# Kernel tuning notes

Measured on AMD Instinct MI355X. Metric: run time of the kernel, lower is better.

## Reference

```python
import jax, jax.numpy as jnp
import numpy as np

EMBED_DIM = 1024
NUM_HEADS = 16
HEAD_DIM = EMBED_DIM // NUM_HEADS
WINDOW = 3
N_RAND = 3
BLOCK = 64
BATCH = 2
SEQ = 2048


def _bigbird_mask(seq_len: int) -> np.ndarray:
    """Global + sliding-window + random block mask. True = attend.
    Deterministic (fixed numpy seed) stand-in for np.random.choice in the
    original; the mask is data-independent so it is a compile-time constant."""
    nb = -(-seq_len // BLOCK)  # ceil division
    mask = np.zeros((seq_len, seq_len), dtype=bool)
    g = min(BLOCK, seq_len)
    mask[:g, :] = True  # global rows
    mask[:, :g] = True  # global cols
    blk = np.arange(seq_len) // BLOCK
    # sliding window: block distance <= WINDOW (matches start/end block loop)
    mask |= np.abs(blk[:, None] - blk[None, :]) <= WINDOW
    rng = np.random.RandomState(0)
    for b in range(1, nb):
        avail = [x for x in range(1, nb) if abs(x - b) > WINDOW]
        if avail:
            sel = rng.choice(avail, size=min(N_RAND, len(avail)), replace=False)
            s0, s1 = b * BLOCK, min(seq_len, (b + 1) * BLOCK)
            for rb in sel:
                mask[s0:s1, rb * BLOCK:min(seq_len, (rb + 1) * BLOCK)] = True
    return mask


def setup_inputs() -> dict:
    key = jax.random.key(0)
    ks = jax.random.split(key, 9)
    E = EMBED_DIM
    std = E ** -0.5
    return {
        "hidden_states": jax.random.normal(ks[0], (BATCH, SEQ, E), jnp.float32),
        "wq": jax.random.normal(ks[1], (E, E), jnp.float32) * std,
        "bq": jnp.zeros((E,), jnp.float32),
        "wk": jax.random.normal(ks[2], (E, E), jnp.float32) * std,
        "bk": jnp.zeros((E,), jnp.float32),
        "wv": jax.random.normal(ks[3], (E, E), jnp.float32) * std,
        "bv": jnp.zeros((E,), jnp.float32),
        "wo": jax.random.normal(ks[4], (E, E), jnp.float32) * std,
        "bo": jnp.zeros((E,), jnp.float32),
    }


def reference(hidden_states, wq, bq, wk, bk, wv, bv, wo, bo):
    B, S, E = hidden_states.shape
    D = HEAD_DIM
    scale = D ** -0.5

    def proj(w, b):  # (B,S,E) -> (B,H,S,D)
        return (hidden_states @ w.T + b).reshape(B, S, NUM_HEADS, D).transpose(0, 2, 1, 3)

    q = proj(wq, bq)
    k = proj(wk, bk)
    v = proj(wv, bv)
    scores = jnp.einsum('bhqd,bhkd->bhqk', q, k) * scale  # dense, masked post-hoc (as in source)
    mask = jnp.asarray(_bigbird_mask(S))
    scores = jnp.where(mask[None, None, :, :], scores, -jnp.inf)
    attn = jax.nn.softmax(scores, axis=-1)
    out = jnp.einsum('bhqk,bhkd->bhqd', attn, v)
    out = out.transpose(0, 2, 1, 3).reshape(B, S, E)
    return out @ wo.T + bo
```

## Files before the change

### kernel.cpp

```cpp
#include <hip/hip_runtime.h>
#include <cstdint>
#include <math.h>


#define DEVI __device__ __forceinline__

typedef __bf16 bf16x8 __attribute__((ext_vector_type(8)));
typedef float floatx4 __attribute__((ext_vector_type(4)));
typedef unsigned short u16x8 __attribute__((ext_vector_type(8)));
typedef unsigned short u16x4 __attribute__((ext_vector_type(4)));
typedef unsigned short ushort_t;

typedef const __attribute__((address_space(1))) void* gptr_as1;
typedef __attribute__((address_space(3))) void* lptr_as3;

DEVI ushort_t f2bf(float f) {
  unsigned u = __float_as_uint(f);
  unsigned r = ((u >> 16) & 1u) + 0x7fffu;
  return (ushort_t)((u + r) >> 16);
}

DEVI void lds_load16(void* lds, const void* g) {
  __builtin_amdgcn_global_load_lds((gptr_as1)g, (lptr_as3)lds, 16, 0, 0);
}

DEVI floatx4 mfma16(bf16x8 a, bf16x8 b, floatx4 c) {
  return __builtin_amdgcn_mfma_f32_16x16x32_bf16(a, b, c, 0, 0, 0);
}

#define BARR() do { asm volatile("" ::: "memory"); \
                    __builtin_amdgcn_s_barrier();  \
                    asm volatile("" ::: "memory"); } while (0)
#define LGKM0() asm volatile("s_waitcnt lgkmcnt(0)" ::: "memory")
#define VMC(N) asm volatile("s_waitcnt vmcnt(" #N ")" ::: "memory")

struct MTState { unsigned mt[624]; int mti; };

constexpr unsigned mt_next(MTState& s) {
  if (s.mti >= 624) {
    for (int k = 0; k < 624; ++k) {
      unsigned y = (s.mt[k] & 0x80000000u) | (s.mt[(k + 1) % 624] & 0x7fffffffu);
      unsigned v = s.mt[(k + 397) % 624] ^ (y >> 1);
      if (y & 1u) v ^= 0x9908b0dfu;
      s.mt[k] = v;
    }
    s.mti = 0;
  }
  unsigned y = s.mt[s.mti++];
  y ^= y >> 11;
  y ^= (y << 7) & 0x9d2c5680u;
  y ^= (y << 15) & 0xefc60000u;
  y ^= y >> 18;
  return y;
}

constexpr unsigned mt_interval(MTState& s, unsigned mx) {
  if (mx == 0u) return 0u;
  unsigned msk = mx;
  msk |= msk >> 1; msk |= msk >> 2; msk |= msk >> 4; msk |= msk >> 8; msk |= msk >> 16;
  unsigned v = mt_next(s) & msk;
  while (v > mx) v = mt_next(s) & msk;
  return v;
}

struct MaskPack { unsigned char list[32][32]; int cnt[32]; };

constexpr MaskPack make_pack() {
  unsigned char m[32][32] = {};
  for (int i = 0; i < 32; ++i)
    for (int j = 0; j < 32; ++j) {
      int d = i - j; if (d < 0) d = -d;
      m[i][j] = (i == 0 || j == 0 || d <= 3) ? (unsigned char)1 : (unsigned char)0;
    }
  MTState st{};
  st.mt[0] = 0u;
  for (int i = 1; i < 624; ++i)
    st.mt[i] = 1812433253u * (st.mt[i - 1] ^ (st.mt[i - 1] >> 30)) + (unsigned)i;
  st.mti = 624;
  for (int b = 1; b < 32; ++b) {
    int avail[32] = {}; int n = 0;
    for (int x = 1; x < 32; ++x) {
      int d = x - b; if (d < 0) d = -d;
      if (d > 3) avail[n++] = x;
    }
    if (n == 0) continue;
    int perm[32] = {};
    for (int i = 0; i < n; ++i) perm[i] = i;
    for (int i = n - 1; i > 0; --i) {
      unsigned j = mt_interval(st, (unsigned)i);
      int t = perm[i]; perm[i] = perm[(int)j]; perm[(int)j] = t;
    }
    int take = n < 3 ? n : 3;
    for (int s = 0; s < take; ++s) m[b][avail[perm[s]]] = 1;
  }
  MaskPack P{};
  for (int i = 0; i < 32; ++i) {
    int c = 0;
    for (int j = 0; j < 32; ++j)
      if (m[i][j]) P.list[i][c++] = (unsigned char)j;
    P.cnt[i] = c;
  }
  return P;
}

__constant__ MaskPack MP = make_pack();

__global__ __launch_bounds__(256) void cvt_all(
    const float* __restrict__ hs, const float* __restrict__ wq,
    const float* __restrict__ wk, const float* __restrict__ wv,
    const float* __restrict__ wo,
    ushort_t* __restrict__ hs_bf, ushort_t* __restrict__ wq_bf,
    ushort_t* __restrict__ wk_bf, ushort_t* __restrict__ wv_bf,
    ushort_t* __restrict__ wo_bf) {
  const int i = blockIdx.x * 256 + threadIdx.x;
  const float* s;
  ushort_t* d;
  int j;
  if (i < 1048576) {
    s = hs; d = hs_bf; j = i;
  } else {
    const int t = (i - 1048576) >> 18;
    j = (i - 1048576) & 262143;
    s = t == 0 ? wq : (t == 1 ? wk : (t == 2 ? wv : wo));
    d = t == 0 ? wq_bf : (t == 1 ? wk_bf : (t == 2 ? wv_bf : wo_bf));
  }
  const float4 f = ((const float4*)s)[j];
  u16x4 o;
  o.x = f2bf(f.x); o.y = f2bf(f.y); o.z = f2bf(f.z); o.w = f2bf(f.w);
  ((u16x4*)d)[j] = o;
}

DEVI void stage_half(ushort_t* ldsb, const ushort_t* g, int w, int l) {
  lds_load16(ldsb + w * 1024 + l * 8, g);
  lds_load16(ldsb + w * 1024 + 512 + l * 8, g + 8192);
}

DEVI void rdA(bf16x8 (&a)[4][2], const ushort_t* base, int wm, int li, int quad) {
#pragma unroll
  for (int mi = 0; mi < 4; ++mi) {
    const int rh = wm * 64 + mi * 16 + li;
    const int sw = rh & 7;
#pragma unroll
    for (int ks = 0; ks < 2; ++ks)
      a[mi][ks] = *(const bf16x8*)(base + rh * 64 + (((ks * 4 + quad) ^ sw) << 3));
  }
}

DEVI void rdB(bf16x8 (&b)[2][2], const ushort_t* base, int wn, int li, int quad) {
#pragma unroll
  for (int ni = 0; ni < 2; ++ni) {
    const int rh = wn * 32 + ni * 16 + li;
    const int sw = rh & 7;
#pragma unroll
    for (int ks = 0; ks < 2; ++ks)
      b[ni][ks] = *(const bf16x8*)(base + rh * 64 + (((ks * 4 + quad) ^ sw) << 3));
  }
}

DEVI void mm16(floatx4 (&c)[4][2], const bf16x8 (&a)[4][2], const bf16x8 (&b)[2][2]) {
  __builtin_amdgcn_s_setprio(1);
#pragma unroll
  for (int ks = 0; ks < 2; ++ks)
#pragma unroll
    for (int mi = 0; mi < 4; ++mi)
#pragma unroll
      for (int ni = 0; ni < 2; ++ni)
        c[mi][ni] = mfma16(a[mi][ks], b[ni][ks], c[mi][ni]);
  __builtin_amdgcn_s_setprio(0);
}

__global__ __launch_bounds__(512, 2) void gemm_qkv_fused(
    const ushort_t* __restrict__ A,
    const ushort_t* __restrict__ W0, const ushort_t* __restrict__ W1,
    const ushort_t* __restrict__ W2,
    const float* __restrict__ bq, const float* __restrict__ bk,
    const float* __restrict__ bv,
    ushort_t* __restrict__ Qo, ushort_t* __restrict__ Ko,
    ushort_t* __restrict__ Vt) {
  __shared__ alignas(16) ushort_t LDS[2][2][2][8192];
  const int tid = threadIdx.x;
  const int w = tid >> 6, l = tid & 63, quad = l >> 4, li = l & 15;
  const int wm = w >> 2, wn = w & 3;
  const int bid = blockIdx.x;
  const int swz = (bid & 7) * 24 + (bid >> 3);
  const int m0 = (swz / 12) << 8;
  const int n0g = (swz % 12) << 8;
  const int z = n0g >> 10, n0l = n0g & 1023;
  const ushort_t* Bw = z == 0 ? W0 : (z == 1 ? W1 : W2);
  const float* bias = z == 0 ? bq : (z == 1 ? bk : bv);

  const int rst = w * 16 + (l >> 3);
  const int cst = ((l & 7) ^ (l >> 3)) << 3;
  const ushort_t* gA = A + (size_t)(m0 + rst) * 1024 + cst;
  const ushort_t* gB = Bw + (size_t)(n0l + rst) * 1024 + cst;

  const floatx4 fz = {0.0f, 0.0f, 0.0f, 0.0f};
  floatx4 acc[2][2][4][2];
#pragma unroll
  for (int qm = 0; qm < 2; ++qm)
#pragma unroll
    for (int qn = 0; qn < 2; ++qn)
#pragma unroll
      for (int mi = 0; mi < 4; ++mi)
#pragma unroll
        for (int ni = 0; ni < 2; ++ni) acc[qm][qn][mi][ni] = fz;

  bf16x8 a[4][2], b0[2][2], b1[2][2];

  stage_half(&LDS[0][0][0][0], gA, w, l);
  stage_half(&LDS[0][0][1][0], gA + 131072, w, l);
  stage_half(&LDS[0][1][0][0], gB, w, l);
  stage_half(&LDS[0][1][1][0], gB + 131072, w, l);
  stage_half(&LDS[1][0][0][0], gA + 64, w, l);
  stage_half(&LDS[1][1][0][0], gB + 64, w, l);
  stage_half(&LDS[1][1][1][0], gB + 131072 + 64, w, l);
  VMC(6);
  BARR();

#pragma unroll 1
  for (int it = 0; it < 8; ++it) {
    const bool pf = (it < 7);
    const int o_cy = (2 * it + 1) * 64;
    const int o_x = (2 * it + 2) * 64;
    const int o_y = (2 * it + 3) * 64;

    rdA(a, &LDS[0][0][0][0], wm, li, quad);
    rdB(b0, &LDS[0][1][0][0], wn, li, quad);
    stage_half(&LDS[1][0][1][0], gA + 131072 + o_cy, w, l);
    BARR(); LGKM0();
    mm16(acc[0][0], a, b0);
    BARR();

    rdB(b1, &LDS[0][1][1][0], wn, li, quad);
    if (pf) stage_half(&LDS[0][0][0][0], gA + o_x, w, l);
    BARR(); LGKM0();
    mm16(acc[0][1], a, b1);
    BARR();

    rdA(a, &LDS[0][0][1][0], wm, li, quad);
    if (pf) stage_half(&LDS[0][1][0][0], gB + o_x, w, l);
    BARR(); LGKM0();
    mm16(acc[1][0], a, b0);
    BARR();

    if (pf) stage_half(&LDS[0][1][1][0], gB + 131072 + o_x, w, l);
    BARR(); LGKM0();
    mm16(acc[1][1], a, b1);
    if (pf) { VMC(6); } else { VMC(0); }
    BARR();

    rdA(a, &LDS[1][0][0][0], wm, li, quad);
    rdB(b0, &LDS[1][1][0][0], wn, li, quad);
    if (pf) stage_half(&LDS[0][0][1][0], gA + 131072 + o_x, w, l);
    BARR(); LGKM0();
    mm16(acc[0][0], a, b0);
    BARR();

    rdB(b1, &LDS[1][1][1][0], wn, li, quad);
    if (pf) stage_half(&LDS[1][0][0][0], gA + o_y, w, l);
    BARR(); LGKM0();
    mm16(acc[0][1], a, b1);
    BARR();

    rdA(a, &LDS[1][0][1][0], wm, li, quad);
    if (pf) stage_half(&LDS[1][1][0][0], gB + o_y, w, l);
    BARR(); LGKM0();
    mm16(acc[1][0], a, b0);
    BARR();

    if (pf) stage_half(&LDS[1][1][1][0], gB + 131072 + o_y, w, l);
    BARR(); LGKM0();
    mm16(acc[1][1], a, b1);
    if (pf) { VMC(6); }
    BARR();
  }

#pragma unroll
  for (int Qm = 0; Qm < 2; ++Qm)
#pragma unroll
    for (int Qn = 0; Qn < 2; ++Qn)
#pragma unroll
      for (int ni = 0; ni < 2; ++ni) {
        const int col = n0l + Qn * 128 + wn * 32 + ni * 16 + li;
        const float bb_ = bias[col];
        if (z == 2) {
          const int hh = col >> 6, dd = col & 63;
#pragma unroll
          for (int mi = 0; mi < 4; ++mi) {
            const int row0 = m0 + Qm * 128 + wm * 64 + mi * 16 + quad * 4;
            const int bb = row0 >> 11, s0 = row0 & 2047;
            u16x4 pk;
#pragma unroll
            for (int r = 0; r < 4; ++r) pk[r] = f2bf(acc[Qm][Qn][mi][ni][r] + bb_);
            *(u16x4*)(Vt + (size_t)((bb * 16 + hh) * 64 + dd) * 2048 + s0) = pk;
          }
        } else {
          ushort_t* Co = (z == 0) ? Qo : Ko;
#pragma unroll
          for (int mi = 0; mi < 4; ++mi)
#pragma unroll
            for (int r = 0; r < 4; ++r) {
              const int row = m0 + Qm * 128 + wm * 64 + mi * 16 + quad * 4 + r;
              Co[(size_t)row * 1024 + col] = f2bf(acc[Qm][Qn][mi][ni][r] + bb_);
            }
        }
      }
}

__global__ __launch_bounds__(256) void gemm_o64(
    const ushort_t* __restrict__ A, const ushort_t* __restrict__ W,
    const float* __restrict__ bias, float* __restrict__ C) {
  constexpr int N = 1024, K = 1024;
  __shared__ alignas(16) ushort_t As[64 * 32];
  __shared__ alignas(16) ushort_t Bs[128 * 32];
  const int tid = threadIdx.x;
  const int w = tid >> 6, l = tid & 63, quad = l >> 4, li = l & 15;
  const int m0 = blockIdx.x * 64, n0 = blockIdx.y * 128;
  const int wm = (w >> 1) * 32, wn = (w & 1) * 64;

  const int lofA = w * 512 + l * 8;
  const int rA = lofA >> 5, cA = lofA & 31;
  const int lofB0 = (w * 2 + 0) * 512 + l * 8;
  const int lofB1 = (w * 2 + 1) * 512 + l * 8;
  const int rB0 = lofB0 >> 5, cB0 = lofB0 & 31;
  const int rB1 = lofB1 >> 5, cB1 = lofB1 & 31;
  const ushort_t* gA = A + (size_t)(m0 + rA) * K + cA;
  const ushort_t* gB0 = W + (size_t)(n0 + rB0) * K + cB0;
  const ushort_t* gB1 = W + (size_t)(n0 + rB1) * K + cB1;

  const floatx4 fzero = {0.0f, 0.0f, 0.0f, 0.0f};
  floatx4 acc[2][4];
#pragma unroll
  for (int i = 0; i < 2; ++i)
#pragma unroll
    for (int j = 0; j < 4; ++j) acc[i][j] = fzero;

  for (int k0 = 0; k0 < K; k0 += 32) {
    lds_load16(As + lofA, gA + k0);
    lds_load16(Bs + lofB0, gB0 + k0);
    lds_load16(Bs + lofB1, gB1 + k0);
    __syncthreads();
    bf16x8 af[2], bfr[4];
#pragma unroll
    for (int mi = 0; mi < 2; ++mi)
      af[mi] = *(const bf16x8*)(As + (wm + mi * 16 + li) * 32 + quad * 8);
#pragma unroll
    for (int ni = 0; ni < 4; ++ni)
      bfr[ni] = *(const bf16x8*)(Bs + (wn + ni * 16 + li) * 32 + quad * 8);
#pragma unroll
    for (int mi = 0; mi < 2; ++mi)
#pragma unroll
      for (int ni = 0; ni < 4; ++ni)
        acc[mi][ni] = mfma16(af[mi], bfr[ni], acc[mi][ni]);
    __syncthreads();
  }

#pragma unroll
  for (int ni = 0; ni < 4; ++ni) {
    const int col = n0 + wn + ni * 16 + li;
    const float bv = bias[col];
#pragma unroll
    for (int mi = 0; mi < 2; ++mi) {
#pragma unroll
      for (int r = 0; r < 4; ++r) {
        const int row = m0 + wm + mi * 16 + quad * 4 + r;
        C[(size_t)row * N + col] = acc[mi][ni][r] + bv;
      }
    }
  }
}

__global__ __launch_bounds__(256) void attn_kernel(
    const ushort_t* __restrict__ Q, const ushort_t* __restrict__ Kg,
    const ushort_t* __restrict__ Vtg, ushort_t* __restrict__ O) {
  __shared__ alignas(16) ushort_t Kls[64 * 72];
  __shared__ alignas(16) ushort_t Vls[64 * 72];
  __shared__ alignas(16) ushort_t Ps[4][16 * 72];

  const int tid = threadIdx.x;
  const int w = tid >> 6, l = tid & 63, quad = l >> 4, li = l & 15;
  const int hb = blockIdx.x, qb = blockIdx.y;
  const int h = hb & 15, b = hb >> 4;
  const size_t qoff = (size_t)b * 2048 * 1024 + (size_t)h * 64;
  const size_t vtoff = (size_t)hb * 64 * 2048;

  unsigned lw[8];
#pragma unroll
  for (int j = 0; j < 8; ++j) lw[j] = ((const unsigned*)(MP.list[qb]))[j];
  const int nact = MP.cnt[qb];
  auto roll = [&]() -> int {
    const int kb = (int)(lw[0] & 255u);
#pragma unroll
    for (int j = 0; j < 7; ++j) lw[j] = (lw[j] >> 8) | (lw[j + 1] << 24);
    lw[7] >>= 8;
    return kb;
  };

  const int qrow = qb * 64 + w * 16 + li;
  bf16x8 aq0 = *(const bf16x8*)(Q + qoff + (size_t)qrow * 1024 + quad * 8);
  bf16x8 aq1 = *(const bf16x8*)(Q + qoff + (size_t)qrow * 1024 + 32 + quad * 8);
#pragma unroll
  for (int j = 0; j < 8; ++j) {
    aq0[j] = (__bf16)((float)aq0[j] * 0.125f);
    aq1[j] = (__bf16)((float)aq1[j] * 0.125f);
  }

  const floatx4 fzero = {0.0f, 0.0f, 0.0f, 0.0f};
  floatx4 o_acc[4];
  float lp[4];
#pragma unroll
  for (int nt = 0; nt < 4; ++nt) o_acc[nt] = fzero;
#pragma unroll
  for (int r = 0; r < 4; ++r) lp[r] = 0.0f;

  const int r0 = w * 16 + (l >> 3);
  const int r1 = r0 + 8;
  const int cb = (l & 7) * 8;
  const ushort_t* kg0 = Kg + qoff + (size_t)r0 * 1024 + cb;
  const ushort_t* kg1 = Kg + qoff + (size_t)r1 * 1024 + cb;
  const ushort_t* vg0 = Vtg + vtoff + (size_t)r0 * 2048 + cb;
  const ushort_t* vg1 = Vtg + vtoff + (size_t)r1 * 2048 + cb;
  ushort_t* kd0 = Kls + r0 * 72 + cb;
  ushort_t* kd1 = Kls + r1 * 72 + cb;
  ushort_t* vd0 = Vls + r0 * 72 + cb;
  ushort_t* vd1 = Vls + r1 * 72 + cb;
  ushort_t* PsW = Ps[w];

  int kb = roll();
  {
    const u16x8 a0 = *(const u16x8*)(kg0 + (size_t)kb * 65536);
    const u16x8 a1 = *(const u16x8*)(kg1 + (size_t)kb * 65536);
    const u16x8 b0 = *(const u16x8*)(vg0 + kb * 64);
    const u16x8 b1 = *(const u16x8*)(vg1 + kb * 64);
    *(u16x8*)kd0 = a0; *(u16x8*)kd1 = a1;
    *(u16x8*)vd0 = b0; *(u16x8*)vd1 = b1;
  }

  for (int i = 0; i < nact; ++i) {
    const int kbn = (i + 1 < nact) ? roll() : 0;
    __syncthreads();

    floatx4 s[4];
#pragma unroll
    for (int nt = 0; nt < 4; ++nt) {
      const bf16x8 bk0 = *(const bf16x8*)(Kls + (nt * 16 + li) * 72 + quad * 8);
      const bf16x8 bk1 = *(const bf16x8*)(Kls + (nt * 16 + li) * 72 + 32 + quad * 8);
      s[nt] = mfma16(aq1, bk1, mfma16(aq0, bk0, fzero));
    }

#pragma unroll
    for (int nt = 0; nt < 4; ++nt)
#pragma unroll
      for (int r = 0; r < 4; ++r) {
        const float e = __expf(s[nt][r]);
        lp[r] += e;
        PsW[(quad * 4 + r) * 72 + nt * 16 + li] = f2bf(e);
      }

#pragma unroll
    for (int c = 0; c < 2; ++c) {
      const bf16x8 pa = *(const bf16x8*)(PsW + li * 72 + c * 32 + quad * 8);
#pragma unroll
      for (int nt = 0; nt < 4; ++nt) {
        const bf16x8 vb = *(const bf16x8*)(Vls + (nt * 16 + li) * 72 + c * 32 + quad * 8);
        o_acc[nt] = mfma16(pa, vb, o_acc[nt]);
      }
    }

    __syncthreads();
    if (i + 1 < nact) {
      const u16x8 a0 = *(const u16x8*)(kg0 + (size_t)kbn * 65536);
      const u16x8 a1 = *(const u16x8*)(kg1 + (size_t)kbn * 65536);
      const u16x8 b0 = *(const u16x8*)(vg0 + kbn * 64);
      const u16x8 b1 = *(const u16x8*)(vg1 + kbn * 64);
      *(u16x8*)kd0 = a0; *(u16x8*)kd1 = a1;
      *(u16x8*)vd0 = b0; *(u16x8*)vd1 = b1;
    }
  }

#pragma unroll
  for (int stp = 1; stp <= 8; stp <<= 1)
#pragma unroll
    for (int r = 0; r < 4; ++r) lp[r] += __shfl_xor(lp[r], stp);

#pragma unroll
  for (int r = 0; r < 4; ++r) {
    const float rinv = 1.0f / lp[r];
#pragma unroll
    for (int nt = 0; nt < 4; ++nt) {
      const float ov = o_acc[nt][r] * rinv;
      O[qoff + (size_t)(qb * 64 + w * 16 + quad * 4 + r) * 1024 + nt * 16 + li] = f2bf(ov);
    }
  }
}

extern "C" void kernel_launch(void* const* d_in, const int* in_sizes, int n_in,
                              void* d_out, int out_size, void* d_ws, size_t ws_size,
                              hipStream_t stream) {
  const float* hs = (const float*)d_in[0];
  const float* wq = (const float*)d_in[1];
  const float* bq = (const float*)d_in[2];
  const float* wk = (const float*)d_in[3];
  const float* bk = (const float*)d_in[4];
  const float* wv = (const float*)d_in[5];
  const float* bv = (const float*)d_in[6];
  const float* wo = (const float*)d_in[7];
  const float* bo = (const float*)d_in[8];
  float* out = (float*)d_out;

  char* ws = (char*)d_ws;
  ushort_t* hs_bf = (ushort_t*)(ws);
  ushort_t* wq_bf = (ushort_t*)(ws + (8ull << 20));
  ushort_t* wk_bf = (ushort_t*)(ws + (10ull << 20));
  ushort_t* wv_bf = (ushort_t*)(ws + (12ull << 20));
  ushort_t* wo_bf = (ushort_t*)(ws + (14ull << 20));
  ushort_t* Qb = (ushort_t*)(ws + (16ull << 20));
  ushort_t* Kb = (ushort_t*)(ws + (24ull << 20));
  ushort_t* Vt = (ushort_t*)(ws + (32ull << 20));
  ushort_t* AO = hs_bf;

  cvt_all<<<8192, 256, 0, stream>>>(hs, wq, wk, wv, wo,
                                    hs_bf, wq_bf, wk_bf, wv_bf, wo_bf);

  gemm_qkv_fused<<<192, 512, 0, stream>>>(hs_bf, wq_bf, wk_bf, wv_bf,
                                          bq, bk, bv, Qb, Kb, Vt);

  dim3 ga(32, 32, 1);
  attn_kernel<<<ga, 256, 0, stream>>>(Qb, Kb, Vt, AO);

  dim3 go(64, 8, 1);
  gemm_o64<<<go, 256, 0, stream>>>(AO, wo_bf, bo, out);
}
```

Baseline: 184.3 us.

## Split global query block attention across three partial CTAs plus combine kernel

Query block 0 is a global row that attends to all 32 key blocks, roughly three times the work of the other query blocks, so its CTAs form a long tail. The attention grid now runs that block as three partial CTAs over 11, 11 and 10 key blocks. Each partial writes unnormalized fp32 outputs and row sums to workspace, and a new small kernel adds them and normalizes. Key block indices are now read directly from the mask list instead of a register-shifted list. The cost is an extra kernel launch plus fp32 scratch traffic, and the split relies on the softmax having no max subtraction so partial sums can simply be added.

```diff
diff --git a/kernel.cpp b/kernel.cpp
--- a/kernel.cpp
+++ b/kernel.cpp
@@ -372,29 +372,25 @@
 
 __global__ __launch_bounds__(256) void attn_kernel(
     const ushort_t* __restrict__ Q, const ushort_t* __restrict__ Kg,
-    const ushort_t* __restrict__ Vtg, ushort_t* __restrict__ O) {
+    const ushort_t* __restrict__ Vtg, ushort_t* __restrict__ O,
+    float* __restrict__ OP, float* __restrict__ LP) {
   __shared__ alignas(16) ushort_t Kls[64 * 72];
   __shared__ alignas(16) ushort_t Vls[64 * 72];
   __shared__ alignas(16) ushort_t Ps[4][16 * 72];
 
   const int tid = threadIdx.x;
   const int w = tid >> 6, l = tid & 63, quad = l >> 4, li = l & 15;
-  const int hb = blockIdx.x, qb = blockIdx.y;
+  const int hb = blockIdx.x;
+  const int y = blockIdx.y;
+  const bool partial = (y >= 31);
+  const int qb = partial ? 0 : (y + 1);
+  const int p = partial ? (y - 31) : 0;
+  const int base = p * 11;
+  const int nact = partial ? (32 - base < 11 ? 32 - base : 11) : MP.cnt[qb];
+
   const int h = hb & 15, b = hb >> 4;
   const size_t qoff = (size_t)b * 2048 * 1024 + (size_t)h * 64;
   const size_t vtoff = (size_t)hb * 64 * 2048;
-
-  unsigned lw[8];
-#pragma unroll
-  for (int j = 0; j < 8; ++j) lw[j] = ((const unsigned*)(MP.list[qb]))[j];
-  const int nact = MP.cnt[qb];
-  auto roll = [&]() -> int {
-    const int kb = (int)(lw[0] & 255u);
-#pragma unroll
-    for (int j = 0; j < 7; ++j) lw[j] = (lw[j] >> 8) | (lw[j + 1] << 24);
-    lw[7] >>= 8;
-    return kb;
-  };
 
   const int qrow = qb * 64 + w * 16 + li;
   bf16x8 aq0 = *(const bf16x8*)(Q + qoff + (size_t)qrow * 1024 + quad * 8);
@@ -426,7 +422,7 @@
   ushort_t* vd1 = Vls + r1 * 72 + cb;
   ushort_t* PsW = Ps[w];
 
-  int kb = roll();
+  int kb = MP.list[qb][base];
   {
     const u16x8 a0 = *(const u16x8*)(kg0 + (size_t)kb * 65536);
     const u16x8 a1 = *(const u16x8*)(kg1 + (size_t)kb * 65536);
@@ -437,7 +433,7 @@
   }
 
   for (int i = 0; i < nact; ++i) {
-    const int kbn = (i + 1 < nact) ? roll() : 0;
+    const int kbn = (i + 1 < nact) ? (int)MP.list[qb][base + i + 1] : 0;
     __syncthreads();
 
     floatx4 s[4];
@@ -483,14 +479,42 @@
 #pragma unroll
     for (int r = 0; r < 4; ++r) lp[r] += __shfl_xor(lp[r], stp);
 
-#pragma unroll
-  for (int r = 0; r < 4; ++r) {
-    const float rinv = 1.0f / lp[r];
-#pragma unroll
-    for (int nt = 0; nt < 4; ++nt) {
-      const float ov = o_acc[nt][r] * rinv;
-      O[qoff + (size_t)(qb * 64 + w * 16 + quad * 4 + r) * 1024 + nt * 16 + li] = f2bf(ov);
-    }
+  if (!partial) {
+#pragma unroll
+    for (int r = 0; r < 4; ++r) {
+      const float rinv = 1.0f / lp[r];
+#pragma unroll
+      for (int nt = 0; nt < 4; ++nt) {
+        const float ov = o_acc[nt][r] * rinv;
+        O[qoff + (size_t)(qb * 64 + w * 16 + quad * 4 + r) * 1024 + nt * 16 + li] = f2bf(ov);
+      }
+    }
+  } else {
+    float* O32 = OP + (size_t)(hb * 3 + p) * 4096;
+    float* LPp = LP + (hb * 3 + p) * 64;
+#pragma unroll
+    for (int r = 0; r < 4; ++r) {
+      const int row = w * 16 + quad * 4 + r;
+#pragma unroll
+      for (int nt = 0; nt < 4; ++nt)
+        O32[row * 64 + nt * 16 + li] = o_acc[nt][r];
+      if (li == 0) LPp[row] = lp[r];
+    }
+  }
+}
+
+__global__ __launch_bounds__(256) void combine_qb0(
+    const float* __restrict__ OP, const float* __restrict__ LP,
+    ushort_t* __restrict__ O) {
+  const int hb = blockIdx.x;
+  const int b = hb >> 4, h = hb & 15;
+  const float* o0 = OP + (size_t)hb * 3 * 4096;
+  const float* l0 = LP + hb * 3 * 64;
+  for (int idx = threadIdx.x; idx < 4096; idx += 256) {
+    const int q = idx >> 6, d = idx & 63;
+    const float s = o0[idx] + o0[4096 + idx] + o0[8192 + idx];
+    const float lsum = l0[q] + l0[64 + q] + l0[128 + q];
+    O[(size_t)b * 2048 * 1024 + (size_t)q * 1024 + h * 64 + d] = f2bf(s / lsum);
   }
 }
 
@@ -518,6 +542,9 @@
   ushort_t* Kb = (ushort_t*)(ws + (24ull << 20));
   ushort_t* Vt = (ushort_t*)(ws + (32ull << 20));
   ushort_t* AO = hs_bf;
+  float* OP = (float*)(ws + (10ull << 20));
+  float* LP = (float*)(ws + (10ull << 20) + (2ull << 20));
+  LP = (float*)((char*)OP + 32 * 3 * 4096 * sizeof(float));
 
   cvt_all<<<8192, 256, 0, stream>>>(hs, wq, wk, wv, wo,
                                     hs_bf, wq_bf, wk_bf, wv_bf, wo_bf);
@@ -525,8 +552,10 @@
   gemm_qkv_fused<<<192, 512, 0, stream>>>(hs_bf, wq_bf, wk_bf, wv_bf,
                                           bq, bk, bv, Qb, Kb, Vt);
 
-  dim3 ga(32, 32, 1);
-  attn_kernel<<<ga, 256, 0, stream>>>(Qb, Kb, Vt, AO);
+  dim3 ga(32, 34, 1);
+  attn_kernel<<<ga, 256, 0, stream>>>(Qb, Kb, Vt, AO, OP, LP);
+
+  combine_qb0<<<32, 256, 0, stream>>>(OP, LP, AO);
 
   dim3 go(64, 8, 1);
   gemm_o64<<<go, 256, 0, stream>>>(AO, wo_bf, bo, out);
```

Result: no change. 183.0 us (-0.7%).
